# Optimization experiments

Measured on AMD Instinct MI355X. Metric: run time of the kernel, lower is better.

The kernel has to match this reference:

```python
import jax, jax.numpy as jnp
import numpy as np

B, T, D, H = 8, 2048, 1024, 16
HD = D // H          # head_dim = 64
SC = H               # scales = n_heads = 16
DECAY_MIN, DECAY_MAX = 0.3, 0.99


def setup_inputs() -> dict:
    key = jax.random.key(0)
    k_x, k_in, k_mix, k_gw, k_gb, k_out = jax.random.split(key, 6)
    x = jax.random.normal(k_x, (B, T, D), dtype=jnp.float32)
    pad_mask = jnp.zeros((B, T), dtype=bool)  # True = PAD
    inv = 1.0 / np.sqrt(D)
    W_in = jax.random.uniform(k_in, (D, D), jnp.float32, -inv, inv)
    W_out = jax.random.uniform(k_out, (D, D), jnp.float32, -inv, inv)
    W_gate = jax.random.uniform(k_gw, (D, D), jnp.float32, -inv, inv)
    b_gate = jax.random.uniform(k_gb, (D,), jnp.float32, -inv, inv)
    state_mix = jax.random.normal(k_mix, (H, SC, HD), jnp.float32) / np.sqrt(HD)
    p = jnp.linspace(DECAY_MIN, DECAY_MAX, SC)
    logit_decay = jnp.tile(jnp.log(p / (1.0 - p))[None, :], (H, 1))  # [H, SC]
    return {"x": x, "pad_mask": pad_mask, "W_in": W_in, "state_mix": state_mix,
            "logit_decay": logit_decay, "W_gate": W_gate, "b_gate": b_gate,
            "W_out": W_out}


def reference(x, pad_mask, W_in, state_mix, logit_decay, W_gate, b_gate, W_out):
    Bc, Tc, Dc = x.shape
    Hc, Sc, Hd = state_mix.shape
    h = (x @ W_in.T).reshape(Bc, Tc, Hc, Hd)          # [B,T,H,Hd]
    decays = jax.nn.sigmoid(logit_decay)              # [H,SC]
    keep = 1.0 - pad_mask.astype(x.dtype)             # [B,T], 1 where not PAD

    def step(S, inp):
        ht, mt = inp                                  # [B,H,Hd], [B]
        S = (decays[None, :, :, None] * S + ht[:, :, None, :]) \
            * mt[:, None, None, None]                 # [B,H,SC,Hd]
        read = jnp.einsum('bhsd,hsd->bhd', S, state_mix)
        return S, read

    S0 = jnp.zeros((Bc, Hc, Sc, Hd), dtype=x.dtype)
    _, reads = jax.lax.scan(step, S0, (h.transpose(1, 0, 2, 3), keep.T))
    y = reads.transpose(1, 0, 2, 3).reshape(Bc, Tc, Dc)
    g = jax.nn.sigmoid(x @ W_gate.T + b_gate)
    y = g * y + (1.0 - g) * x
    return y @ W_out.T
```

## Files before the change

kernel.cpp:

```cpp
#include <hip/hip_runtime.h>

#define B_  8
#define T_  2048
#define D_  1024
#define H_  16
#define HD_ 64
#define SC_ 16
#define NC_ 32
#define CT_ 64

typedef __attribute__((ext_vector_type(8))) short short8;
typedef __attribute__((ext_vector_type(4))) float f32x4;

__device__ inline unsigned short f2bf(float f) {
  union { float f; unsigned u; } v; v.f = f;
  unsigned r = v.u + 0x7FFFu + ((v.u >> 16) & 1u);
  return (unsigned short)(r >> 16);
}
__device__ inline float bf2f(unsigned short b) {
  union { unsigned u; float f; } v; v.u = ((unsigned)b) << 16; return v.f;
}

__device__ inline void gl_lds16(const unsigned short* g, unsigned short* l) {
  __builtin_amdgcn_global_load_lds(
      (const __attribute__((address_space(1))) unsigned int*)(g),
      (__attribute__((address_space(3))) unsigned int*)(l), 16, 0, 0);
}

__global__ void conv_f32_bf16(const float* __restrict__ in,
                              unsigned short* __restrict__ out, int n4) {
  int i = blockIdx.x * 256 + threadIdx.x;
  if (i >= n4) return;
  float4 v = ((const float4*)in)[i];
  ushort4 o;
  o.x = f2bf(v.x); o.y = f2bf(v.y); o.z = f2bf(v.z); o.w = f2bf(v.w);
  ((ushort4*)out)[i] = o;
}

template<int MODE>
__global__ __launch_bounds__(256, 2)
void gemm_bt(const unsigned short* __restrict__ A,
             const unsigned short* __restrict__ Bt,
             void* __restrict__ C1, void* __restrict__ C2,
             const float* __restrict__ bgate,
             int M, int N, int K) {
  __shared__ unsigned short As[128 * 64];
  __shared__ unsigned short Bs[128 * 64];
  const int tid  = threadIdx.x;
  const int lane = tid & 63;
  const int w    = tid >> 6;
  const int wm   = w >> 1, wn = w & 1;
  const int l15  = lane & 15, l4 = lane >> 4;
  const int srow   = lane >> 3;
  const int schunk = (lane & 7) ^ srow;
  const int nbn  = N >> 7;
  const int nwg  = gridDim.x;
  int bid = blockIdx.x;
  int b2 = ((nwg & 7) == 0) ? ((bid & 7) * (nwg >> 3) + (bid >> 3)) : bid;
  const int bm = (b2 / nbn) << 7;
  const int bn = (b2 % nbn) << 7;

  f32x4 acc[4][4] = {};

  for (int k0 = 0; k0 < K; k0 += 64) {
#pragma unroll
    for (int i = 0; i < 4; ++i) {
      int q = (w << 2) + i;
      int r = (q << 3) + srow;
      gl_lds16(A  + (size_t)(bm + r) * K + k0 + (schunk << 3), As + (q << 9));
      gl_lds16(Bt + (size_t)(bn + r) * K + k0 + (schunk << 3), Bs + (q << 9));
    }
    __syncthreads();
#pragma unroll
    for (int ks = 0; ks < 2; ++ks) {
      short8 af[4], bf[4];
#pragma unroll
      for (int i = 0; i < 4; ++i) {
        int ra = (wm << 6) + (i << 4) + l15;
        int kc = (ks << 2) + l4;
        af[i] = *(const short8*)(&As[ra * 64 + ((kc ^ (ra & 7)) << 3)]);
        int rb = (wn << 6) + (i << 4) + l15;
        bf[i] = *(const short8*)(&Bs[rb * 64 + ((kc ^ (rb & 7)) << 3)]);
      }
#pragma unroll
      for (int mi = 0; mi < 4; ++mi)
#pragma unroll
        for (int ni = 0; ni < 4; ++ni)
          acc[mi][ni] = __builtin_amdgcn_mfma_f32_16x16x32_bf16(
              af[mi], bf[ni], acc[mi][ni], 0, 0, 0);
    }
    __syncthreads();
  }

  const int rbase = bm + (wm << 6) + (l4 << 2);
  const bool is_gate = (MODE == 2) && (bn >= 1024);
  void* dst = is_gate ? C2 : C1;
  const int cb = is_gate ? (bn - 1024) : bn;
  const int cbase = cb + (wn << 6) + l15;
  const int CN = (MODE == 2) ? 1024 : N;
  float bgv[4];
  if (is_gate) {
#pragma unroll
    for (int ni = 0; ni < 4; ++ni) bgv[ni] = bgate[cbase + (ni << 4)];
  }
#pragma unroll
  for (int mi = 0; mi < 4; ++mi)
#pragma unroll
    for (int ni = 0; ni < 4; ++ni)
#pragma unroll
      for (int r = 0; r < 4; ++r) {
        size_t row = rbase + (mi << 4) + r;
        int col = cbase + (ni << 4);
        if (MODE == 0) {
          ((float*)dst)[row * CN + col] = acc[mi][ni][r];
        } else if (is_gate) {
          float g = 1.f / (1.f + __expf(-(acc[mi][ni][r] + bgv[ni])));
          ((unsigned short*)dst)[row * CN + col] = f2bf(g);
        } else {
          ((unsigned short*)dst)[row * CN + col] = f2bf(acc[mi][ni][r]);
        }
      }
}

__device__ inline bool chunk_has_pad(const unsigned char* pp) {
  const unsigned long long* p8 = (const unsigned long long*)pp;
  unsigned long long v = 0;
#pragma unroll
  for (int i = 0; i < CT_ / 8; ++i) v |= p8[i];
  return v != 0ull;
}

__global__ void scan_pass1(const unsigned short* __restrict__ hb,
                           const unsigned char* __restrict__ pad,
                           const float* __restrict__ ldec,
                           float* __restrict__ Schunk,
                           float* __restrict__ akeep) {
  int gid = blockIdx.x * 256 + threadIdx.x;
  int d  = gid & 63;
  int hh = (gid >> 6) & 15;
  int c  = (gid >> 10) & (NC_ - 1);
  int b  = gid >> 15;
  float dec[SC_], S[SC_];
#pragma unroll
  for (int s = 0; s < SC_; ++s) {
    dec[s] = 1.f / (1.f + __expf(-ldec[hh * SC_ + s]));
    S[s] = 0.f;
  }
  const int t0 = c * CT_;
  const unsigned short* hp = hb + (size_t)(b * T_ + t0) * D_ + hh * HD_ + d;
  const unsigned char* pp = pad + b * T_ + t0;
  bool anypad = chunk_has_pad(pp);
  if (!anypad) {
    for (int t = 0; t < CT_; ++t) {
      float ht = bf2f(*hp); hp += D_;
#pragma unroll
      for (int s = 0; s < SC_; ++s) S[s] = dec[s] * S[s] + ht;
    }
  } else {
    for (int t = 0; t < CT_; ++t) {
      float ht = bf2f(*hp); hp += D_;
      float k = pp[t] ? 0.f : 1.f;
#pragma unroll
      for (int s = 0; s < SC_; ++s) S[s] = (dec[s] * S[s] + ht) * k;
    }
  }
  size_t base = ((size_t)((b * NC_ + c) * H_ + hh) * SC_) * HD_ + d;
#pragma unroll
  for (int s = 0; s < SC_; ++s) Schunk[base + s * HD_] = S[s];
  if (hh == 0 && d == 0) akeep[b * NC_ + c] = anypad ? 0.f : 1.f;
}

__global__ void scan_combine(float* __restrict__ Schunk,
                             const float* __restrict__ akeep,
                             const float* __restrict__ ldec) {
  int gid = blockIdx.x * 256 + threadIdx.x;
  int d  = gid & 63;
  int s  = (gid >> 6) & 15;
  int hh = (gid >> 10) & 15;
  int b  = gid >> 14;
  float dec  = 1.f / (1.f + __expf(-ldec[hh * SC_ + s]));
  float dpow = __powf(dec, (float)CT_);
  float carry = 0.f;
  for (int c = 0; c < NC_; ++c) {
    size_t idx = ((size_t)((b * NC_ + c) * H_ + hh) * SC_ + s) * HD_ + d;
    float e = Schunk[idx];
    Schunk[idx] = carry;
    float Ac = (akeep[b * NC_ + c] != 0.f) ? dpow : 0.f;
    carry = Ac * carry + e;
  }
}

__global__ void scan_pass2(const unsigned short* __restrict__ hb,
                           const unsigned char* __restrict__ pad,
                           const float* __restrict__ ldec,
                           const float* __restrict__ mix,
                           const float* __restrict__ Sstart,
                           const unsigned short* __restrict__ gb,
                           unsigned short* __restrict__ xy) {
  int gid = blockIdx.x * 256 + threadIdx.x;
  int d  = gid & 63;
  int hh = (gid >> 6) & 15;
  int c  = (gid >> 10) & (NC_ - 1);
  int b  = gid >> 15;
  float dec[SC_], mx[SC_], S[SC_];
  size_t sbase = ((size_t)((b * NC_ + c) * H_ + hh) * SC_) * HD_ + d;
#pragma unroll
  for (int s = 0; s < SC_; ++s) {
    dec[s] = 1.f / (1.f + __expf(-ldec[hh * SC_ + s]));
    mx[s]  = mix[(hh * SC_ + s) * HD_ + d];
    S[s]   = Sstart[sbase + s * HD_];
  }
  const int t0 = c * CT_;
  const int col = hh * HD_ + d;
  size_t off = (size_t)(b * T_ + t0) * D_ + col;
  const unsigned char* pp = pad + b * T_ + t0;
  bool anypad = chunk_has_pad(pp);
  if (!anypad) {
    for (int t = 0; t < CT_; ++t, off += D_) {
      float ht = bf2f(hb[off]);
      float rd = 0.f;
#pragma unroll
      for (int s = 0; s < SC_; ++s) {
        S[s] = dec[s] * S[s] + ht;
        rd  += mx[s] * S[s];
      }
      float g  = bf2f(gb[off]);
      float xv = bf2f(xy[off]);
      xy[off] = f2bf(fmaf(g, rd - xv, xv));
    }
  } else {
    for (int t = 0; t < CT_; ++t, off += D_) {
      float ht = bf2f(hb[off]);
      float k = pp[t] ? 0.f : 1.f;
      float rd = 0.f;
#pragma unroll
      for (int s = 0; s < SC_; ++s) {
        S[s] = (dec[s] * S[s] + ht) * k;
        rd  += mx[s] * S[s];
      }
      float g  = bf2f(gb[off]);
      float xv = bf2f(xy[off]);
      xy[off] = f2bf(fmaf(g, rd - xv, xv));
    }
  }
}

extern "C" void kernel_launch(void* const* d_in, const int* in_sizes, int n_in,
                              void* d_out, int out_size, void* d_ws, size_t ws_size,
                              hipStream_t stream) {
  const float* x          = (const float*)d_in[0];
  const unsigned char* pm = (const unsigned char*)d_in[1];
  const float* W_in       = (const float*)d_in[2];
  const float* smix       = (const float*)d_in[3];
  const float* ldec       = (const float*)d_in[4];
  const float* W_gate     = (const float*)d_in[5];
  const float* b_gate     = (const float*)d_in[6];
  const float* W_out      = (const float*)d_in[7];
  float* out = (float*)d_out;
  char* ws = (char*)d_ws;

  const int NX = B_ * T_ * D_;
  const int NW = D_ * D_;

  unsigned short* xb    = (unsigned short*)(ws);
  unsigned short* wbin  = (unsigned short*)(ws + 33554432);
  unsigned short* wbgt  = (unsigned short*)(ws + 35651584);
  unsigned short* wbout = (unsigned short*)(ws + 37748736);
  unsigned short* hb    = (unsigned short*)(ws + 39845888);
  float* Schunk         = (float*)(ws + 73400320);
  float* akeep          = (float*)(ws + 90177536);
  unsigned short* gb    = (unsigned short*)d_out;

  conv_f32_bf16<<<NX / 1024, 256, 0, stream>>>(x, xb, NX / 4);
  conv_f32_bf16<<<NW / 1024, 256, 0, stream>>>(W_in,   wbin,  NW / 4);
  conv_f32_bf16<<<NW / 1024, 256, 0, stream>>>(W_gate, wbgt,  NW / 4);
  conv_f32_bf16<<<NW / 1024, 256, 0, stream>>>(W_out,  wbout, NW / 4);

  const int M = B_ * T_;

  dim3 gg2((M / 128) * (2048 / 128));
  gemm_bt<2><<<gg2, 256, 0, stream>>>(xb, wbin, hb, gb, b_gate, M, 2048, D_);

  dim3 sg1(B_ * NC_ * H_ * HD_ / 256);
  dim3 sgc(B_ * H_ * SC_ * HD_ / 256);
  scan_pass1 <<<sg1, 256, 0, stream>>>(hb, pm, ldec, Schunk, akeep);
  scan_combine<<<sgc, 256, 0, stream>>>(Schunk, akeep, ldec);
  scan_pass2 <<<sg1, 256, 0, stream>>>(hb, pm, ldec, smix, Schunk, gb, xb);

  dim3 gg((M / 128) * (D_ / 128));
  gemm_bt<0><<<gg, 256, 0, stream>>>(xb, wbout, out, nullptr, nullptr, M, D_, D_);
}
```

Baseline: 197.2 us.

## Replace 128x128 GEMM with 256x256 triple-buffered pipelined bf16 GEMM

Replaces the single-buffered 128x128 tile GEMM with a 256x256 tile, 512-thread kernel. It uses a three-stage LDS ring with global_load_lds prefetch two K-steps ahead, explicit vmcnt waits and one barrier per step. It also uses K=32 slices with a new XOR swizzle, and raises wave priority around the MFMA blocks. The goal is to hide global load latency and improve operand reuse. The cost is one block per CU, 96KB of LDS and more accumulator registers per thread.

```diff
diff --git a/kernel.cpp b/kernel.cpp
--- a/kernel.cpp
+++ b/kernel.cpp
@@ -38,65 +38,106 @@
 }
 
 template<int MODE>
-__global__ __launch_bounds__(256, 2)
-void gemm_bt(const unsigned short* __restrict__ A,
+__global__ __launch_bounds__(512, 1)
+void gemm256(const unsigned short* __restrict__ A,
              const unsigned short* __restrict__ Bt,
              void* __restrict__ C1, void* __restrict__ C2,
              const float* __restrict__ bgate,
              int M, int N, int K) {
-  __shared__ unsigned short As[128 * 64];
-  __shared__ unsigned short Bs[128 * 64];
+  __shared__ unsigned short lds[3 * 16384];
   const int tid  = threadIdx.x;
   const int lane = tid & 63;
   const int w    = tid >> 6;
-  const int wm   = w >> 1, wn = w & 1;
+  const int wm   = w >> 2, wn = w & 3;
   const int l15  = lane & 15, l4 = lane >> 4;
-  const int srow   = lane >> 3;
-  const int schunk = (lane & 7) ^ srow;
-  const int nbn  = N >> 7;
-  const int nwg  = gridDim.x;
+  const int srow = lane >> 2;
+  const int gc   = (lane & 3) ^ ((lane >> 3) & 3);
+  const int aslot = l4 ^ ((l15 >> 1) & 3);
+
+  const int nbn = N >> 8;
+  const int nwg = gridDim.x;
   int bid = blockIdx.x;
-  int b2 = ((nwg & 7) == 0) ? ((bid & 7) * (nwg >> 3) + (bid >> 3)) : bid;
-  const int bm = (b2 / nbn) << 7;
-  const int bn = (b2 % nbn) << 7;
-
-  f32x4 acc[4][4] = {};
-
-  for (int k0 = 0; k0 < K; k0 += 64) {
-#pragma unroll
-    for (int i = 0; i < 4; ++i) {
-      int q = (w << 2) + i;
-      int r = (q << 3) + srow;
-      gl_lds16(A  + (size_t)(bm + r) * K + k0 + (schunk << 3), As + (q << 9));
-      gl_lds16(Bt + (size_t)(bn + r) * K + k0 + (schunk << 3), Bs + (q << 9));
-    }
-    __syncthreads();
-#pragma unroll
-    for (int ks = 0; ks < 2; ++ks) {
-      short8 af[4], bf[4];
-#pragma unroll
-      for (int i = 0; i < 4; ++i) {
-        int ra = (wm << 6) + (i << 4) + l15;
-        int kc = (ks << 2) + l4;
-        af[i] = *(const short8*)(&As[ra * 64 + ((kc ^ (ra & 7)) << 3)]);
-        int rb = (wn << 6) + (i << 4) + l15;
-        bf[i] = *(const short8*)(&Bs[rb * 64 + ((kc ^ (rb & 7)) << 3)]);
-      }
-#pragma unroll
-      for (int mi = 0; mi < 4; ++mi)
-#pragma unroll
-        for (int ni = 0; ni < 4; ++ni)
-          acc[mi][ni] = __builtin_amdgcn_mfma_f32_16x16x32_bf16(
-              af[mi], bf[ni], acc[mi][ni], 0, 0, 0);
-    }
-    __syncthreads();
-  }
-
-  const int rbase = bm + (wm << 6) + (l4 << 2);
+  int b2 = (bid & 7) * (nwg >> 3) + (bid >> 3);
+  const int bm = (b2 / nbn) << 8;
+  const int bn = (b2 % nbn) << 8;
+
+  const unsigned short* Ag0 = A  + (size_t)(bm + (w * 2 + 0) * 16 + srow) * K + gc * 8;
+  const unsigned short* Ag1 = A  + (size_t)(bm + (w * 2 + 1) * 16 + srow) * K + gc * 8;
+  const unsigned short* Bg0 = Bt + (size_t)(bn + (w * 2 + 0) * 16 + srow) * K + gc * 8;
+  const unsigned short* Bg1 = Bt + (size_t)(bn + (w * 2 + 1) * 16 + srow) * K + gc * 8;
+
+#define STAGE_A(t, buf) do {                                      \
+    size_t _g = (size_t)(t) * 32;                                 \
+    gl_lds16(Ag0 + _g, &lds[(buf) * 16384 + (w * 2 + 0) * 512]);  \
+    gl_lds16(Ag1 + _g, &lds[(buf) * 16384 + (w * 2 + 1) * 512]);  \
+  } while (0)
+#define STAGE_B(t, buf) do {                                      \
+    size_t _g = (size_t)(t) * 32;                                 \
+    gl_lds16(Bg0 + _g, &lds[(buf) * 16384 + 8192 + (w * 2 + 0) * 512]); \
+    gl_lds16(Bg1 + _g, &lds[(buf) * 16384 + 8192 + (w * 2 + 1) * 512]); \
+  } while (0)
+
+  f32x4 acc[8][4] = {};
+  const int nt = K >> 5;
+
+  STAGE_A(0, 0); STAGE_B(0, 0);
+  STAGE_A(1, 1); STAGE_B(1, 1);
+  asm volatile("s_waitcnt vmcnt(4)" ::: "memory");
+  asm volatile("s_barrier" ::: "memory");
+
+  int bufc = 0;
+  int bufs = 2;
+  for (int t = 0; t < nt; ++t) {
+    const unsigned short* Ab = &lds[bufc * 16384];
+    const unsigned short* Bb = Ab + 8192;
+    const bool do_stage = (t + 2 < nt);
+    short8 afr[4], bfr[4];
+
+    if (do_stage) STAGE_A(t + 2, bufs);
+#pragma unroll
+    for (int ni = 0; ni < 4; ++ni)
+      bfr[ni] = *(const short8*)(Bb + (wn * 64 + ni * 16 + l15) * 32 + aslot * 8);
+#pragma unroll
+    for (int mi = 0; mi < 4; ++mi)
+      afr[mi] = *(const short8*)(Ab + (wm * 128 + mi * 16 + l15) * 32 + aslot * 8);
+    __builtin_amdgcn_s_setprio(1);
+#pragma unroll
+    for (int mi = 0; mi < 4; ++mi)
+#pragma unroll
+      for (int ni = 0; ni < 4; ++ni)
+        acc[mi][ni] = __builtin_amdgcn_mfma_f32_16x16x32_bf16(
+            afr[mi], bfr[ni], acc[mi][ni], 0, 0, 0);
+    __builtin_amdgcn_s_setprio(0);
+
+    if (do_stage) STAGE_B(t + 2, bufs);
+#pragma unroll
+    for (int mi = 0; mi < 4; ++mi)
+      afr[mi] = *(const short8*)(Ab + (wm * 128 + (mi + 4) * 16 + l15) * 32 + aslot * 8);
+    __builtin_amdgcn_s_setprio(1);
+#pragma unroll
+    for (int mi = 0; mi < 4; ++mi)
+#pragma unroll
+      for (int ni = 0; ni < 4; ++ni)
+        acc[mi + 4][ni] = __builtin_amdgcn_mfma_f32_16x16x32_bf16(
+            afr[mi], bfr[ni], acc[mi + 4][ni], 0, 0, 0);
+    __builtin_amdgcn_s_setprio(0);
+
+    if (t < nt - 2)
+      asm volatile("s_waitcnt vmcnt(4)" ::: "memory");
+    else if (t == nt - 2)
+      asm volatile("s_waitcnt vmcnt(0)" ::: "memory");
+    asm volatile("s_barrier" ::: "memory");
+    bufc = (bufc == 2) ? 0 : bufc + 1;
+    bufs = (bufs == 2) ? 0 : bufs + 1;
+  }
+#undef STAGE_A
+#undef STAGE_B
+
+  const int rbase = bm + wm * 128 + (l4 << 2);
   const bool is_gate = (MODE == 2) && (bn >= 1024);
   void* dst = is_gate ? C2 : C1;
   const int cb = is_gate ? (bn - 1024) : bn;
-  const int cbase = cb + (wn << 6) + l15;
+  const int cbase = cb + wn * 64 + l15;
   const int CN = (MODE == 2) ? 1024 : N;
   float bgv[4];
   if (is_gate) {
@@ -104,7 +145,7 @@
     for (int ni = 0; ni < 4; ++ni) bgv[ni] = bgate[cbase + (ni << 4)];
   }
 #pragma unroll
-  for (int mi = 0; mi < 4; ++mi)
+  for (int mi = 0; mi < 8; ++mi)
 #pragma unroll
     for (int ni = 0; ni < 4; ++ni)
 #pragma unroll
@@ -278,8 +319,8 @@
 
   const int M = B_ * T_;
 
-  dim3 gg2((M / 128) * (2048 / 128));
-  gemm_bt<2><<<gg2, 256, 0, stream>>>(xb, wbin, hb, gb, b_gate, M, 2048, D_);
+  dim3 gg2((M / 256) * (2048 / 256));
+  gemm256<2><<<gg2, 512, 0, stream>>>(xb, wbin, hb, gb, b_gate, M, 2048, D_);
 
   dim3 sg1(B_ * NC_ * H_ * HD_ / 256);
   dim3 sgc(B_ * H_ * SC_ * HD_ / 256);
@@ -287,6 +328,6 @@
   scan_combine<<<sgc, 256, 0, stream>>>(Schunk, akeep, ldec);
   scan_pass2 <<<sg1, 256, 0, stream>>>(hb, pm, ldec, smix, Schunk, gb, xb);
 
-  dim3 gg((M / 128) * (D_ / 128));
-  gemm_bt<0><<<gg, 256, 0, stream>>>(xb, wbout, out, nullptr, nullptr, M, D_, D_);
-}
+  dim3 gg((M / 256) * (D_ / 256));
+  gemm256<0><<<gg, 512, 0, stream>>>(xb, wbout, out, nullptr, nullptr, M, D_, D_);
+}
```

Measured after the change: 228.4 us. 15.8% more time.
